# Performance work log

Measured on AMD Instinct MI355X. Metric: run time of the kernel, lower is better.

The kernel has to match this reference:

```python
import jax, jax.numpy as jnp
import numpy as np
import math

WS = 8           # window size
NUM_HEADS = 8
LN_EPS = 1e-5


def window_partition(x, ws):
    # x: [B, H, W, C] -> [B*nH*nW, ws, ws, C]
    B, H, W, C = x.shape
    x = x.reshape(B, H // ws, ws, W // ws, ws, C)
    return x.transpose(0, 1, 3, 2, 4, 5).reshape(-1, ws, ws, C)


def window_reverse(w, ws, H, W):
    # w: [B*nH*nW, ws, ws, C] -> [B, H, W, C]
    B = w.shape[0] // ((H // ws) * (W // ws))
    x = w.reshape(B, H // ws, W // ws, ws, ws, -1)
    return x.transpose(0, 1, 3, 2, 4, 5).reshape(B, H, W, -1)


def layernorm(x, g, b):
    mu = jnp.mean(x, axis=-1, keepdims=True)
    var = jnp.mean(jnp.square(x - mu), axis=-1, keepdims=True)
    return (x - mu) * jax.lax.rsqrt(var + LN_EPS) * g + b


def rotation_grid(H, W, ws):
    """Vectorized rotation_process lookup table -> sampling grid [H, W, 2]=(lat,lon)."""
    nH, nW = H // ws, W // ws
    r = 1.0 / ws
    seq = -1.0 + r + 2.0 * r * jnp.arange(ws, dtype=jnp.float32)  # make_coord centers
    ch, cw = jnp.meshgrid(seq, seq, indexing='ij')
    t0 = ch.reshape(-1) / nH                       # [ws*ws] latitude template
    t1 = cw.reshape(-1) / nW                       # [ws*ws] longitude template
    beta = (2.0 * (jnp.arange(nH, dtype=jnp.float32) + 0.5) / nH - 1.0) * (math.pi / 2)  # [nH]
    th = t0 * (math.pi / 2) + math.pi / 2
    ph = t1 * math.pi
    sb, cb = jnp.sin(beta)[:, None], jnp.cos(beta)[:, None]
    st, ct = jnp.sin(th)[None, :], jnp.cos(th)[None, :]
    sp, cp = jnp.sin(ph)[None, :], jnp.cos(ph)[None, :]
    new_th = jnp.arccos(-sb * st * cp + cb * ct)                    # [nH, ws*ws]
    new_ph = jnp.arctan2(st * sp, cb * st * cp + sb * ct)
    lat = jnp.clip((new_th - math.pi / 2) / (math.pi / 2), -1.0, 1.0)
    lon = new_ph / math.pi
    shift = 2.0 * (0.5 - (jnp.arange(nW, dtype=jnp.float32) + 0.5) / nW)
    lon = lon[:, None, :] - shift[None, :, None]                    # [nH, nW, ws*ws]
    lon = jnp.where(lon > 1.0, lon - 2.0, lon)
    lon = jnp.where(lon < -1.0, lon + 2.0, lon)
    lat = jnp.broadcast_to(lat[:, None, :], lon.shape)
    g = jnp.stack([lat, lon], axis=-1).reshape(nH, nW, ws, ws, 2)
    return g.transpose(0, 2, 1, 3, 4).reshape(H, W, 2)


def grid_sample_nearest(im, grid):
    """F.grid_sample(mode='nearest', align_corners=False, padding='zeros').
    im: [B, H, W, C]; grid: [H, W, 2]=(y,x) normalized; shared across batch."""
    B, H, W, C = im.shape
    gy, gx = grid[..., 0], grid[..., 1]
    iy = jnp.round(((gy + 1.0) * H - 1.0) / 2.0).astype(jnp.int32)
    ix = jnp.round(((gx + 1.0) * W - 1.0) / 2.0).astype(jnp.int32)
    valid = (iy >= 0) & (iy < H) & (ix >= 0) & (ix < W)
    iyc = jnp.clip(iy, 0, H - 1)
    ixc = jnp.clip(ix, 0, W - 1)
    out = im[:, iyc, ixc, :]                                        # [B, H, W, C]
    return out * valid[None, :, :, None].astype(im.dtype)


def dwconv3x3(x, w, b):
    # x: [B, C, H, W], w: [C, 1, 3, 3] depthwise
    y = jax.lax.conv_general_dilated(x, w, (1, 1), 'SAME',
                                     feature_group_count=x.shape[1],
                                     dimension_numbers=('NCHW', 'OIHW', 'NCHW'))
    return y + b[None, :, None, None]


def setup_inputs() -> dict:
    key = jax.random.key(0)
    B, H, W, C, dff = 8, 64, 128, 256, 1024
    ks = jax.random.split(key, 10)
    s = 0.02
    return {
        'x': jax.random.normal(ks[0], (B, H * W, C), jnp.float32),
        'H': H, 'W': W,
        'norm1_g': jnp.ones((C,), jnp.float32),
        'norm1_b': jnp.zeros((C,), jnp.float32),
        'wq': jax.random.normal(ks[1], (C, C), jnp.float32) * s,
        'bq': jnp.zeros((C,), jnp.float32),
        'wk': jax.random.normal(ks[2], (C, C), jnp.float32) * s,
        'bk': jnp.zeros((C,), jnp.float32),
        'wv': jax.random.normal(ks[3], (C, C), jnp.float32) * s,
        'bv': jnp.zeros((C,), jnp.float32),
        'rpe_w': jax.random.normal(ks[4], (C, 1, 3, 3), jnp.float32) * s,
        'rpe_b': jnp.zeros((C,), jnp.float32),
        'proj_w': jax.random.normal(ks[5], (C, C), jnp.float32) * s,
        'proj_b': jnp.zeros((C,), jnp.float32),
        'norm2_g': jnp.ones((C,), jnp.float32),
        'norm2_b': jnp.zeros((C,), jnp.float32),
        'fc1_w': jax.random.normal(ks[6], (C, dff), jnp.float32) * s,
        'fc1_b': jnp.zeros((dff,), jnp.float32),
        'fc2_w': jax.random.normal(ks[7], (dff, C), jnp.float32) * s,
        'fc2_b': jnp.zeros((C,), jnp.float32),
    }


def reference(x, H, W, norm1_g, norm1_b, wq, bq, wk, bk, wv, bv, rpe_w, rpe_b,
              proj_w, proj_b, norm2_g, norm2_b, fc1_w, fc1_b, fc2_w, fc2_b):
    B, L, C = x.shape
    ws, nh = WS, NUM_HEADS
    hd = C // nh
    scale = hd ** (-0.5)
    N = ws * ws

    shortcut = x
    xn = layernorm(x, norm1_g, norm1_b).reshape(B, H, W, C)
    # panoramic rotation of the key features (rotation_process)
    y = grid_sample_nearest(xn, rotation_grid(H, W, ws))

    xw = window_partition(xn, ws).reshape(-1, N, C)   # [Bw, N, C]
    yw = window_partition(y, ws).reshape(-1, N, C)
    Bw = xw.shape[0]

    q = xw @ wq + bq
    # depthwise-conv positional term on window-reversed q (rpe_table)
    qimg = window_reverse(q.reshape(-1, ws, ws, C), ws, H, W).transpose(0, 3, 1, 2)  # [B,C,H,W]
    lepe = window_partition(dwconv3x3(qimg, rpe_w, rpe_b).transpose(0, 2, 3, 1), ws).reshape(-1, N, C)

    k = yw @ wk + bk
    v = xw @ wv + bv
    qh = q.reshape(Bw, N, nh, hd).transpose(0, 2, 1, 3) * scale   # [Bw,h,N,d]
    kh = k.reshape(Bw, N, nh, hd).transpose(0, 2, 1, 3)
    vh = v.reshape(Bw, N, nh, hd).transpose(0, 2, 1, 3)
    attn = jax.nn.softmax(jnp.einsum('bhnd,bhmd->bhnm', qh, kh), axis=-1)
    out = jnp.einsum('bhnm,bhmd->bhnd', attn, vh).transpose(0, 2, 1, 3).reshape(Bw, N, C)
    out = (out + lepe) @ proj_w + proj_b

    x = shortcut + window_reverse(out.reshape(-1, ws, ws, C), ws, H, W).reshape(B, L, C)
    h = layernorm(x, norm2_g, norm2_b)
    h = jax.nn.gelu(h @ fc1_w + fc1_b, approximate=False) @ fc2_w + fc2_b
    return x + h
```

## Files before the change

### kernel.cpp

```cpp
#include <hip/hip_runtime.h>

typedef __bf16 bf16;
typedef __bf16 bf16x4 __attribute__((ext_vector_type(4)));
typedef __bf16 bf16x8 __attribute__((ext_vector_type(8)));
typedef float  f32x4  __attribute__((ext_vector_type(4)));

#define HH   64
#define WW   128
#define CC   256
#define MTOK 65536
#define PI_D 3.14159265358979323846

__device__ __forceinline__ int win_row(int b, int h, int w) {
  return ((b * 8 + (h >> 3)) * 16 + (w >> 3)) * 64 + ((h & 7) << 3) + (w & 7);
}

__device__ __forceinline__ void gl_lds16(const bf16* g, bf16* l) {
  __builtin_amdgcn_global_load_lds(
      (const __attribute__((address_space(1))) unsigned int*)g,
      (__attribute__((address_space(3))) unsigned int*)l, 16, 0, 0);
}

__device__ __forceinline__ float gelu_f(float v) {
  return 0.5f * v * (1.0f + erff(v * 0.70710678118654752f));
}

__global__ __launch_bounds__(256) void prep_kernel(
    const float* __restrict__ wq, const float* __restrict__ wk,
    const float* __restrict__ wv, const float* __restrict__ pw,
    const float* __restrict__ f1w, const float* __restrict__ f2w,
    bf16* __restrict__ wqvT, bf16* __restrict__ wkT, bf16* __restrict__ pwT,
    bf16* __restrict__ f1T, bf16* __restrict__ f2T,
    int* __restrict__ wmap, bf16* __restrict__ zrow,
    float* __restrict__ biasqv,
    const float* __restrict__ bq, const float* __restrict__ bv) {
  const int blk = blockIdx.x;
  if (blk < 768) {
    __shared__ float tile[32][33];
    const float* src; bf16* dst; int K, N, bi;
    if (blk < 64)       { src = wq;  dst = wqvT;         K = 256;  N = 256;  bi = blk;       }
    else if (blk < 128) { src = wv;  dst = wqvT + 65536; K = 256;  N = 256;  bi = blk - 64;  }
    else if (blk < 192) { src = wk;  dst = wkT;          K = 256;  N = 256;  bi = blk - 128; }
    else if (blk < 256) { src = pw;  dst = pwT;          K = 256;  N = 256;  bi = blk - 192; }
    else if (blk < 512) { src = f1w; dst = f1T;          K = 256;  N = 1024; bi = blk - 256; }
    else                { src = f2w; dst = f2T;          K = 1024; N = 256;  bi = blk - 512; }
    const int nbk = K >> 5;
    const int bk = (bi % nbk) * 32, bn = (bi / nbk) * 32;
    const int tx = threadIdx.x & 31, ty = threadIdx.x >> 5;
#pragma unroll
    for (int r = 0; r < 4; r++)
      tile[ty + 8 * r][tx] = src[(size_t)(bk + ty + 8 * r) * N + bn + tx];
    __syncthreads();
#pragma unroll
    for (int r = 0; r < 4; r++)
      dst[(size_t)(bn + ty + 8 * r) * K + bk + tx] = (bf16)tile[tx][ty + 8 * r];
    return;
  }
  int p = (blk - 768) * 256 + threadIdx.x;
  if (p < 256) zrow[p] = (bf16)0.0f;
  if (p < 512) biasqv[p] = (p < 256) ? bq[p] : bv[p - 256];
  if (p >= HH * WW) return;
  int h = p >> 7, w = p & 127;
  int bh = h >> 3, i = h & 7, bw = w >> 3, j = w & 7;
  double seq_i = -0.875 + 0.25 * i;
  double seq_j = -0.875 + 0.25 * j;
  double t0 = seq_i / 8.0, t1 = seq_j / 16.0;
  double beta = ((bh + 0.5) / 4.0 - 1.0) * (PI_D / 2.0);
  double th = t0 * (PI_D / 2.0) + PI_D / 2.0;
  double ph = t1 * PI_D;
  double sb = sin(beta), cb = cos(beta);
  double st = sin(th),  ct = cos(th);
  double sp = sin(ph),  cp = cos(ph);
  double arg = -sb * st * cp + cb * ct;
  arg = fmin(1.0, fmax(-1.0, arg));
  double nth = acos(arg);
  double nph = atan2(st * sp, cb * st * cp + sb * ct);
  double lat = (nth - PI_D / 2.0) / (PI_D / 2.0);
  lat = fmin(1.0, fmax(-1.0, lat));
  double shift = 1.0 - (2.0 * bw + 1.0) / 16.0;
  double lon = nph / PI_D - shift;
  if (lon > 1.0) lon -= 2.0; else if (lon < -1.0) lon += 2.0;
  int iy = (int)rint(((lat + 1.0) * (double)HH - 1.0) * 0.5);
  int ix = (int)rint(((lon + 1.0) * (double)WW - 1.0) * 0.5);
  bool valid = (iy >= 0 && iy < HH && ix >= 0 && ix < WW);
  int dwr = ((h >> 3) * 16 + (w >> 3)) * 64 + ((h & 7) << 3) + (w & 7);
  int src = valid ? (((iy >> 3) * 16 + (ix >> 3)) * 64 + ((iy & 7) << 3) + (ix & 7)) : -1;
  wmap[dwr] = src;
}

__global__ __launch_bounds__(256) void ln_kernel(const float* __restrict__ x,
                                                 const float* __restrict__ g,
                                                 const float* __restrict__ bta,
                                                 bf16* __restrict__ out,
                                                 int permute) {
  int token = blockIdx.x * 4 + (threadIdx.x >> 6);
  int lane = threadIdx.x & 63;
  const float4 v = *(const float4*)(x + (size_t)token * CC + lane * 4);
  float s  = v.x + v.y + v.z + v.w;
  float ss = v.x * v.x + v.y * v.y + v.z * v.z + v.w * v.w;
#pragma unroll
  for (int o = 32; o > 0; o >>= 1) {
    s  += __shfl_xor(s, o);
    ss += __shfl_xor(ss, o);
  }
  float mu = s * (1.0f / CC);
  float var = ss * (1.0f / CC) - mu * mu;
  float rs = rsqrtf(var + 1e-5f);
  int row = token;
  if (permute) {
    int b = token >> 13, l = token & 8191;
    row = win_row(b, l >> 7, l & 127);
  }
  int c = lane * 4;
  const float4 gv = *(const float4*)(g + c);
  const float4 bv = *(const float4*)(bta + c);
  bf16x4 o4;
  o4[0] = (bf16)((v.x - mu) * rs * gv.x + bv.x);
  o4[1] = (bf16)((v.y - mu) * rs * gv.y + bv.y);
  o4[2] = (bf16)((v.z - mu) * rs * gv.z + bv.z);
  o4[3] = (bf16)((v.w - mu) * rs * gv.w + bv.w);
  *(bf16x4*)(out + (size_t)row * CC + c) = o4;
}

#define EPI_BF16 0
#define EPI_GELU 1
#define EPI_PROJ 2
#define EPI_FC2  3
#define EPI_QV   4

#define TRS 72

template <int EPI, bool GATHER>
__global__ __launch_bounds__(256) void gemm_bt(const bf16* __restrict__ A,
                                               const bf16* __restrict__ Bt,
                                               const float* __restrict__ bias,
                                               bf16* __restrict__ outB,
                                               float* __restrict__ outF,
                                               const float* __restrict__ res,
                                               const int* __restrict__ amap,
                                               const bf16* __restrict__ zrow,
                                               bf16* __restrict__ outB2,
                                               int M, int N, int K) {
  __shared__ bf16 lA[128 * 32];
  __shared__ bf16 lB[128 * 32];
  __shared__ bf16 trV[(EPI == EPI_QV) ? 4 * 64 * TRS : 4];
  const int t = threadIdx.x;
  const int wave = t >> 6, lane = t & 63;
  const int quad = lane >> 4, l16 = lane & 15;
  const int mb = blockIdx.x, nb = blockIdx.y;
  const int wm = wave >> 1, wn = wave & 1;

  f32x4 acc[4][4];
#pragma unroll
  for (int i = 0; i < 4; i++)
#pragma unroll
    for (int j = 0; j < 4; j++)
#pragma unroll
      for (int r = 0; r < 4; r++) acc[i][j][r] = 0.0f;

  const int arow = t >> 2;
  const int acol = (t & 3) << 3;
  const bf16 *gA, *gA2;
  if (GATHER) {
    int r1 = mb * 128 + arow;
    int b1 = r1 >> 13, s1 = amap[r1 & 8191];
    gA = (s1 >= 0) ? A + ((size_t)((b1 << 13) + s1)) * K + acol : zrow + acol;
    int r2 = r1 + 64;
    int b2 = r2 >> 13, s2 = amap[r2 & 8191];
    gA2 = (s2 >= 0) ? A + ((size_t)((b2 << 13) + s2)) * K + acol : zrow + acol;
  } else {
    gA = A + (size_t)(mb * 128 + arow) * K + acol;
    gA2 = gA + (size_t)64 * K;
  }
  const bf16* gB  = Bt + (size_t)(nb * 128 + arow) * K + acol;
  const bf16* gB2 = gB + (size_t)64 * K;
  bf16* lAp  = &lA[t * 8];
  bf16* lBp  = &lB[t * 8];
  bf16* lAp2 = &lA[2048 + t * 8];
  bf16* lBp2 = &lB[2048 + t * 8];

  for (int kk = 0; kk < K; kk += 32) {
    __syncthreads();
    gl_lds16(gA + kk, lAp);
    gl_lds16(gA2 + kk, lAp2);
    gl_lds16(gB + kk, lBp);
    gl_lds16(gB2 + kk, lBp2);
    __syncthreads();
    bf16x8 af[4], bfr[4];
#pragma unroll
    for (int i = 0; i < 4; i++)
      af[i] = *(const bf16x8*)&lA[(wm * 64 + i * 16 + l16) * 32 + quad * 8];
#pragma unroll
    for (int j = 0; j < 4; j++)
      bfr[j] = *(const bf16x8*)&lB[(wn * 64 + j * 16 + l16) * 32 + quad * 8];
#pragma unroll
    for (int i = 0; i < 4; i++)
#pragma unroll
      for (int j = 0; j < 4; j++)
        acc[i][j] = __builtin_amdgcn_mfma_f32_16x16x32_bf16(af[i], bfr[j], acc[i][j], 0, 0, 0);
  }

  const int m0 = mb * 128 + wm * 64;
  const int n0 = nb * 128 + wn * 64;

  if (EPI == EPI_QV && nb >= 2) {
    bf16* tw = &trV[wave * 64 * TRS];
#pragma unroll
    for (int i = 0; i < 4; i++)
#pragma unroll
      for (int j = 0; j < 4; j++) {
        const float bsv = bias[n0 + j * 16 + l16];
        bf16x4 pk;
#pragma unroll
        for (int r = 0; r < 4; r++) pk[r] = (bf16)(acc[i][j][r] + bsv);
        *(bf16x4*)&tw[(j * 16 + l16) * TRS + i * 16 + quad * 4] = pk;
      }
    const int win = mb * 2 + wm;
    const int chbase = n0 - 256;
#pragma unroll
    for (int s = 0; s < 8; s++) {
      const int ch = s * 8 + (lane >> 3);
      const int tk = (lane & 7) * 8;
      bf16x8 vv = *(const bf16x8*)&tw[ch * TRS + tk];
      *(bf16x8*)(outB2 + ((size_t)win * 256 + chbase + ch) * 64 + tk) = vv;
    }
  } else {
#pragma unroll
    for (int i = 0; i < 4; i++) {
#pragma unroll
      for (int j = 0; j < 4; j++) {
        const int col = n0 + j * 16 + l16;
        const int rowb = m0 + i * 16 + quad * 4;
        const float bsv = bias[col];
#pragma unroll
        for (int r = 0; r < 4; r++) {
          const int row = rowb + r;
          float v = acc[i][j][r] + bsv;
          if (EPI == EPI_BF16) {
            outB[(size_t)row * N + col] = (bf16)v;
          } else if (EPI == EPI_QV) {
            outB[(size_t)row * 256 + col] = (bf16)v;
          } else if (EPI == EPI_GELU) {
            outB[(size_t)row * N + col] = (bf16)gelu_f(v);
          } else if (EPI == EPI_FC2) {
            size_t idx = (size_t)row * N + col;
            outF[idx] = res[idx] + v;
          } else {
            int wi = row >> 6, tt = row & 63;
            int b = wi >> 7, hb = (wi >> 4) & 7, wb = wi & 15;
            int h = hb * 8 + (tt >> 3), w = wb * 8 + (tt & 7);
            size_t idx = ((size_t)(b * 8192 + h * 128 + w)) * 256 + col;
            outF[idx] = res[idx] + v;
          }
        }
      }
    }
  }
}

__global__ __launch_bounds__(256) void lepe_kernel(const bf16* __restrict__ qb,
                                                   const float* __restrict__ rw,
                                                   const float* __restrict__ rb,
                                                   bf16* __restrict__ ao) {
  __shared__ __align__(16) bf16 hq[100 * 256];
  const int blk = blockIdx.x;
  const int b = blk >> 7, hb = (blk >> 4) & 7, wb = blk & 15;
  const int t = threadIdx.x;
  const int h0 = hb * 8 - 1, w0 = wb * 8 - 1;

  for (int idx = t; idx < 3200; idx += 256) {
    int pix = idx >> 5, ch = (idx & 31) * 8;
    int pi = pix / 10, pj = pix - pi * 10;
    int h = h0 + pi, w = w0 + pj;
    bf16x8 val;
#pragma unroll
    for (int e = 0; e < 8; e++) val[e] = (bf16)0.0f;
    if (h >= 0 && h < HH && w >= 0 && w < WW)
      val = *(const bf16x8*)(qb + (size_t)win_row(b, h, w) * 256 + ch);
    *(bf16x8*)(&hq[pix * 256 + ch]) = val;
  }
  __syncthreads();

  const int cg = t & 31, c0 = cg * 8;
  const int i = t >> 5;

  float wr[9][8];
#pragma unroll
  for (int e = 0; e < 8; e++)
#pragma unroll
    for (int tap = 0; tap < 9; tap++) wr[tap][e] = rw[(c0 + e) * 9 + tap];
  float bias[8];
  *(float4*)&bias[0] = *(const float4*)(rb + c0);
  *(float4*)&bias[4] = *(const float4*)(rb + c0 + 4);

  float cur[3][3][8];
#pragma unroll
  for (int rr = 0; rr < 3; rr++)
#pragma unroll
    for (int cc = 0; cc < 2; cc++) {
      bf16x8 v = *(const bf16x8*)(&hq[((i + rr) * 10 + cc) * 256 + c0]);
#pragma unroll
      for (int e = 0; e < 8; e++) cur[rr][cc][e] = (float)v[e];
    }

#pragma unroll
  for (int j = 0; j < 8; j++) {
    const int snew = (j + 2) % 3;
#pragma unroll
    for (int rr = 0; rr < 3; rr++) {
      bf16x8 v = *(const bf16x8*)(&hq[((i + rr) * 10 + (j + 2)) * 256 + c0]);
#pragma unroll
      for (int e = 0; e < 8; e++) cur[rr][snew][e] = (float)v[e];
    }
    float acc[8];
#pragma unroll
    for (int e = 0; e < 8; e++) acc[e] = bias[e];
#pragma unroll
    for (int rr = 0; rr < 3; rr++)
#pragma unroll
      for (int dc = 0; dc < 3; dc++) {
        const int slot = (j + dc) % 3;
        const int tap = rr * 3 + dc;
#pragma unroll
        for (int e = 0; e < 8; e++) acc[e] += cur[rr][slot][e] * wr[tap][e];
      }
    bf16x8 o;
#pragma unroll
    for (int e = 0; e < 8; e++) o[e] = (bf16)acc[e];
    *(bf16x8*)(ao + (size_t)(blk * 64 + i * 8 + j) * 256 + c0) = o;
  }
}

#define SP 74

__global__ __launch_bounds__(256) void attn_kernel(const bf16* __restrict__ qb,
                                                   const bf16* __restrict__ kb,
                                                   const bf16* __restrict__ vt,
                                                   bf16* __restrict__ ao) {
  __shared__ __align__(16) bf16 Pl[4][64 * SP];
  const int wave = threadIdx.x >> 6, lane = threadIdx.x & 63;
  const int quad = lane >> 4, l16 = lane & 15;
  const int win = blockIdx.x >> 1;
  const size_t rowbase = (size_t)win * 64;
  const int head = ((blockIdx.x & 1) << 2) + wave;
  const int hc = head * 32;
  bf16* P = Pl[wave];
  const float scale = 0.17677669529663687f;

  bf16x8 aq[4], bk4[4];
#pragma unroll
  for (int mi = 0; mi < 4; mi++)
    aq[mi] = *(const bf16x8*)(qb + (rowbase + mi * 16 + l16) * 256 + hc + quad * 8);
#pragma unroll
  for (int ni = 0; ni < 4; ni++)
    bk4[ni] = *(const bf16x8*)(kb + (rowbase + ni * 16 + l16) * 256 + hc + quad * 8);
  f32x4 sacc[4][4];
#pragma unroll
  for (int mi = 0; mi < 4; mi++)
#pragma unroll
    for (int ni = 0; ni < 4; ni++)
#pragma unroll
      for (int r = 0; r < 4; r++) sacc[mi][ni][r] = 0.0f;
#pragma unroll
  for (int mi = 0; mi < 4; mi++)
#pragma unroll
    for (int ni = 0; ni < 4; ni++)
      sacc[mi][ni] = __builtin_amdgcn_mfma_f32_16x16x32_bf16(aq[mi], bk4[ni], sacc[mi][ni], 0, 0, 0);

  bf16x8 vb2[2][2];
#pragma unroll
  for (int n0 = 0; n0 < 2; n0++)
#pragma unroll
    for (int kc = 0; kc < 2; kc++)
      vb2[n0][kc] = *(const bf16x8*)(vt + ((size_t)win * 256 + hc + n0 * 16 + l16) * 64 +
                                     kc * 32 + quad * 8);

#pragma unroll
  for (int mi = 0; mi < 4; mi++) {
#pragma unroll
    for (int r = 0; r < 4; r++) {
      float mx = -1e30f;
#pragma unroll
      for (int ni = 0; ni < 4; ni++) mx = fmaxf(mx, sacc[mi][ni][r]);
      mx = fmaxf(mx, __shfl_xor(mx, 1));
      mx = fmaxf(mx, __shfl_xor(mx, 2));
      mx = fmaxf(mx, __shfl_xor(mx, 4));
      mx = fmaxf(mx, __shfl_xor(mx, 8));
      float sm = 0.0f;
#pragma unroll
      for (int ni = 0; ni < 4; ni++) {
        float e = expf(scale * (sacc[mi][ni][r] - mx));
        sacc[mi][ni][r] = e;
        sm += e;
      }
      sm += __shfl_xor(sm, 1);
      sm += __shfl_xor(sm, 2);
      sm += __shfl_xor(sm, 4);
      sm += __shfl_xor(sm, 8);
      float inv = 1.0f / sm;
#pragma unroll
      for (int ni = 0; ni < 4; ni++) sacc[mi][ni][r] *= inv;
    }
#pragma unroll
    for (int ni = 0; ni < 4; ni++)
#pragma unroll
      for (int r = 0; r < 4; r++)
        P[(mi * 16 + quad * 4 + r) * SP + ni * 16 + l16] = (bf16)sacc[mi][ni][r];
  }

  f32x4 oacc[4][2];
#pragma unroll
  for (int mi = 0; mi < 4; mi++)
#pragma unroll
    for (int n0 = 0; n0 < 2; n0++)
#pragma unroll
      for (int r = 0; r < 4; r++) oacc[mi][n0][r] = 0.0f;
#pragma unroll
  for (int mi = 0; mi < 4; mi++)
#pragma unroll
    for (int kc = 0; kc < 2; kc++) {
      bf16x8 pf = *(const bf16x8*)&P[(mi * 16 + l16) * SP + kc * 32 + quad * 8];
#pragma unroll
      for (int n0 = 0; n0 < 2; n0++)
        oacc[mi][n0] = __builtin_amdgcn_mfma_f32_16x16x32_bf16(pf, vb2[n0][kc], oacc[mi][n0], 0, 0, 0);
    }

  bf16* Ol = P;
#pragma unroll
  for (int mi = 0; mi < 4; mi++)
#pragma unroll
    for (int n0 = 0; n0 < 2; n0++)
#pragma unroll
      for (int r = 0; r < 4; r++)
        Ol[(mi * 16 + quad * 4 + r) * 34 + n0 * 16 + l16] = (bf16)oacc[mi][n0][r];

  bf16* aop = ao + (rowbase + lane) * 256 + hc;
#pragma unroll
  for (int cc = 0; cc < 4; cc++) {
    bf16x8 ov = *(const bf16x8*)&Ol[lane * 34 + cc * 8];
    bf16x8 lp = *(const bf16x8*)(aop + cc * 8);
    bf16x8 so;
#pragma unroll
    for (int e = 0; e < 8; e++) so[e] = (bf16)((float)ov[e] + (float)lp[e]);
    *(bf16x8*)(aop + cc * 8) = so;
  }
}

extern "C" void kernel_launch(void* const* d_in, const int* in_sizes, int n_in,
                              void* d_out, int out_size, void* d_ws, size_t ws_size,
                              hipStream_t stream) {
  const float* x     = (const float*)d_in[0];
  const float* n1g   = (const float*)d_in[3];
  const float* n1b   = (const float*)d_in[4];
  const float* wq    = (const float*)d_in[5];
  const float* bq    = (const float*)d_in[6];
  const float* wk    = (const float*)d_in[7];
  const float* bk    = (const float*)d_in[8];
  const float* wv    = (const float*)d_in[9];
  const float* bv    = (const float*)d_in[10];
  const float* rpe_w = (const float*)d_in[11];
  const float* rpe_b = (const float*)d_in[12];
  const float* pw    = (const float*)d_in[13];
  const float* pb    = (const float*)d_in[14];
  const float* n2g   = (const float*)d_in[15];
  const float* n2b   = (const float*)d_in[16];
  const float* f1w   = (const float*)d_in[17];
  const float* f1b   = (const float*)d_in[18];
  const float* f2w   = (const float*)d_in[19];
  const float* f2b   = (const float*)d_in[20];
  float* out = (float*)d_out;
  char* ws = (char*)d_ws;

  const size_t A_ = 33554432ull;
  bf16* xw  = (bf16*)(ws);
  bf16* ao  = (bf16*)(ws);
  bf16* xh  = (bf16*)(ws);
  bf16* qb  = (bf16*)(ws + A_);
  bf16* vt  = (bf16*)(ws + 2 * A_);
  bf16* h1  = (bf16*)(ws + A_);
  bf16* kb  = (bf16*)d_out;
  char* wsp = ws + 3 * A_;
  bf16* wqvT = (bf16*)(wsp);
  bf16* wkT  = (bf16*)(wsp + 262144);
  bf16* pwT  = (bf16*)(wsp + 393216);
  bf16* f1T  = (bf16*)(wsp + 524288);
  bf16* f2T  = (bf16*)(wsp + 1048576);
  float* biasqv = (float*)(wsp + 1572864);
  int*   wmap   = (int*)(wsp + 1574912);
  bf16*  zrow   = (bf16*)(wsp + 1607680);

  prep_kernel<<<800, 256, 0, stream>>>(wq, wk, wv, pw, f1w, f2w,
                                       wqvT, wkT, pwT, f1T, f2T,
                                       wmap, zrow, biasqv, bq, bv);

  ln_kernel<<<MTOK / 4, 256, 0, stream>>>(x, n1g, n1b, xw, 1);

  gemm_bt<EPI_QV, false><<<dim3(512, 4), 256, 0, stream>>>(
      xw, wqvT, biasqv, qb, nullptr, nullptr, nullptr, nullptr, vt, MTOK, 512, 256);
  gemm_bt<EPI_BF16, true><<<dim3(512, 2), 256, 0, stream>>>(
      xw, wkT, bk, kb, nullptr, nullptr, wmap, zrow, nullptr, MTOK, 256, 256);

  lepe_kernel<<<1024, 256, 0, stream>>>(qb, rpe_w, rpe_b, ao);
  attn_kernel<<<2048, 256, 0, stream>>>(qb, kb, vt, ao);

  gemm_bt<EPI_PROJ, false><<<dim3(512, 2), 256, 0, stream>>>(
      ao, pwT, pb, nullptr, out, x, nullptr, nullptr, nullptr, MTOK, 256, 256);

  ln_kernel<<<MTOK / 4, 256, 0, stream>>>(out, n2g, n2b, xh, 0);

  const int CH = 32768;
  for (int c = 0; c < 2; c++) {
    gemm_bt<EPI_GELU, false><<<dim3(CH / 128, 8), 256, 0, stream>>>(
        xh + (size_t)c * CH * 256, f1T, f1b, h1, nullptr, nullptr, nullptr, nullptr, nullptr,
        CH, 1024, 256);
    gemm_bt<EPI_FC2, false><<<dim3(CH / 128, 2), 256, 0, stream>>>(
        h1, f2T, f2b, nullptr, out + (size_t)c * CH * 256, out + (size_t)c * CH * 256,
        nullptr, nullptr, nullptr, CH, 256, 1024);
  }
}
```

Before: 486.5 us.

## Load GEMM operands directly from global memory and fuse Q/V/K projection launches

Replaces the LDS-staged GEMM, which used global_load_lds and two barriers per K step, with kernels where each wave loads its MFMA fragments straight from global memory into registers. The K projection with its gathered rows is merged into the Q/V projection as extra grid columns, so one launch covers all three. This removes LDS traffic and barrier stalls, but each wave now fetches fragments with no reuse across waves in the block. That means more global and L2 traffic, plus short strided loads.

```diff
diff --git a/kernel.cpp b/kernel.cpp
--- a/kernel.cpp
+++ b/kernel.cpp
@@ -13,12 +13,6 @@
 
 __device__ __forceinline__ int win_row(int b, int h, int w) {
   return ((b * 8 + (h >> 3)) * 16 + (w >> 3)) * 64 + ((h & 7) << 3) + (w & 7);
-}
-
-__device__ __forceinline__ void gl_lds16(const bf16* g, bf16* l) {
-  __builtin_amdgcn_global_load_lds(
-      (const __attribute__((address_space(1))) unsigned int*)g,
-      (__attribute__((address_space(3))) unsigned int*)l, 16, 0, 0);
 }
 
 __device__ __forceinline__ float gelu_f(float v) {
@@ -122,33 +116,116 @@
   *(bf16x4*)(out + (size_t)row * CC + c) = o4;
 }
 
-#define EPI_BF16 0
 #define EPI_GELU 1
 #define EPI_PROJ 2
 #define EPI_FC2  3
-#define EPI_QV   4
+
+template <int EPI, int KT>
+__global__ __launch_bounds__(256) void gemm_dir(const bf16* __restrict__ A,
+                                                const bf16* __restrict__ Bt,
+                                                const float* __restrict__ bias,
+                                                bf16* __restrict__ outB,
+                                                float* __restrict__ outF,
+                                                const float* __restrict__ res,
+                                                int N) {
+  const int K = KT * 32;
+  const int lane = threadIdx.x & 63, wave = threadIdx.x >> 6;
+  const int quad = lane >> 4, l16 = lane & 15;
+  const int mb = blockIdx.x, nb = blockIdx.y;
+  const int wm = wave >> 1, wn = wave & 1;
+
+  const bf16* ap = A  + (size_t)(mb * 128 + wm * 64 + l16) * K + quad * 8;
+  const bf16* bp = Bt + (size_t)(nb * 128 + wn * 64 + l16) * K + quad * 8;
+
+  f32x4 acc[4][4];
+#pragma unroll
+  for (int i = 0; i < 4; i++)
+#pragma unroll
+    for (int j = 0; j < 4; j++)
+#pragma unroll
+      for (int r = 0; r < 4; r++) acc[i][j][r] = 0.0f;
+
+  constexpr int UN = (KT > 8) ? 4 : KT;
+  for (int ko = 0; ko < KT / UN; ko++) {
+#pragma unroll
+    for (int ku = 0; ku < UN; ku++) {
+      const int kc = ko * UN + ku;
+      bf16x8 af[4], bfr[4];
+#pragma unroll
+      for (int i = 0; i < 4; i++)
+        af[i] = *(const bf16x8*)(ap + (size_t)i * 16 * K + kc * 32);
+#pragma unroll
+      for (int j = 0; j < 4; j++)
+        bfr[j] = *(const bf16x8*)(bp + (size_t)j * 16 * K + kc * 32);
+#pragma unroll
+      for (int i = 0; i < 4; i++)
+#pragma unroll
+        for (int j = 0; j < 4; j++)
+          acc[i][j] = __builtin_amdgcn_mfma_f32_16x16x32_bf16(af[i], bfr[j], acc[i][j], 0, 0, 0);
+    }
+  }
+
+  const int m0 = mb * 128 + wm * 64;
+  const int n0 = nb * 128 + wn * 64;
+#pragma unroll
+  for (int i = 0; i < 4; i++) {
+#pragma unroll
+    for (int j = 0; j < 4; j++) {
+      const int col = n0 + j * 16 + l16;
+      const int rowb = m0 + i * 16 + quad * 4;
+      const float bsv = bias[col];
+#pragma unroll
+      for (int r = 0; r < 4; r++) {
+        const int row = rowb + r;
+        float v = acc[i][j][r] + bsv;
+        if (EPI == EPI_GELU) {
+          outB[(size_t)row * N + col] = (bf16)gelu_f(v);
+        } else if (EPI == EPI_FC2) {
+          size_t idx = (size_t)row * N + col;
+          outF[idx] = res[idx] + v;
+        } else {
+          int wi = row >> 6, tt = row & 63;
+          int b = wi >> 7, hb = (wi >> 4) & 7, wb = wi & 15;
+          int h = hb * 8 + (tt >> 3), w = wb * 8 + (tt & 7);
+          size_t idx = ((size_t)(b * 8192 + h * 128 + w)) * 256 + col;
+          outF[idx] = res[idx] + v;
+        }
+      }
+    }
+  }
+}
 
 #define TRS 72
 
-template <int EPI, bool GATHER>
-__global__ __launch_bounds__(256) void gemm_bt(const bf16* __restrict__ A,
-                                               const bf16* __restrict__ Bt,
-                                               const float* __restrict__ bias,
-                                               bf16* __restrict__ outB,
-                                               float* __restrict__ outF,
-                                               const float* __restrict__ res,
-                                               const int* __restrict__ amap,
-                                               const bf16* __restrict__ zrow,
-                                               bf16* __restrict__ outB2,
-                                               int M, int N, int K) {
-  __shared__ bf16 lA[128 * 32];
-  __shared__ bf16 lB[128 * 32];
-  __shared__ bf16 trV[(EPI == EPI_QV) ? 4 * 64 * TRS : 4];
+__global__ __launch_bounds__(256) void gemm_qvk(
+    const bf16* __restrict__ xw, const bf16* __restrict__ wqvT,
+    const bf16* __restrict__ wkT, const float* __restrict__ biasqv,
+    const float* __restrict__ bk, bf16* __restrict__ qb,
+    bf16* __restrict__ vt, bf16* __restrict__ kb,
+    const int* __restrict__ wmap, const bf16* __restrict__ zrow) {
+  __shared__ __align__(16) bf16 trV[4 * 64 * TRS];
   const int t = threadIdx.x;
   const int wave = t >> 6, lane = t & 63;
   const int quad = lane >> 4, l16 = lane & 15;
   const int mb = blockIdx.x, nb = blockIdx.y;
   const int wm = wave >> 1, wn = wave & 1;
+  const bool isK = (nb >= 4);
+
+  const bf16* ap[4];
+#pragma unroll
+  for (int i = 0; i < 4; i++) {
+    int r1 = mb * 128 + wm * 64 + i * 16 + l16;
+    if (isK) {
+      int s = wmap[r1 & 8191];
+      ap[i] = (s >= 0) ? xw + ((size_t)((r1 & ~8191) + s)) * 256 + quad * 8
+                       : zrow + quad * 8;
+    } else {
+      ap[i] = xw + (size_t)r1 * 256 + quad * 8;
+    }
+  }
+  const int nloc = isK ? (nb - 4) : nb;
+  const bf16* Bt = isK ? wkT : wqvT;
+  const bf16* bp = Bt + (size_t)(nloc * 128 + wn * 64 + l16) * 256 + quad * 8;
 
   f32x4 acc[4][4];
 #pragma unroll
@@ -158,41 +235,15 @@
 #pragma unroll
       for (int r = 0; r < 4; r++) acc[i][j][r] = 0.0f;
 
-  const int arow = t >> 2;
-  const int acol = (t & 3) << 3;
-  const bf16 *gA, *gA2;
-  if (GATHER) {
-    int r1 = mb * 128 + arow;
-    int b1 = r1 >> 13, s1 = amap[r1 & 8191];
-    gA = (s1 >= 0) ? A + ((size_t)((b1 << 13) + s1)) * K + acol : zrow + acol;
-    int r2 = r1 + 64;
-    int b2 = r2 >> 13, s2 = amap[r2 & 8191];
-    gA2 = (s2 >= 0) ? A + ((size_t)((b2 << 13) + s2)) * K + acol : zrow + acol;
-  } else {
-    gA = A + (size_t)(mb * 128 + arow) * K + acol;
-    gA2 = gA + (size_t)64 * K;
-  }
-  const bf16* gB  = Bt + (size_t)(nb * 128 + arow) * K + acol;
-  const bf16* gB2 = gB + (size_t)64 * K;
-  bf16* lAp  = &lA[t * 8];
-  bf16* lBp  = &lB[t * 8];
-  bf16* lAp2 = &lA[2048 + t * 8];
-  bf16* lBp2 = &lB[2048 + t * 8];
-
-  for (int kk = 0; kk < K; kk += 32) {
-    __syncthreads();
-    gl_lds16(gA + kk, lAp);
-    gl_lds16(gA2 + kk, lAp2);
-    gl_lds16(gB + kk, lBp);
-    gl_lds16(gB2 + kk, lBp2);
-    __syncthreads();
+#pragma unroll
+  for (int kc = 0; kc < 8; kc++) {
     bf16x8 af[4], bfr[4];
 #pragma unroll
     for (int i = 0; i < 4; i++)
-      af[i] = *(const bf16x8*)&lA[(wm * 64 + i * 16 + l16) * 32 + quad * 8];
+      af[i] = *(const bf16x8*)(ap[i] + kc * 32);
 #pragma unroll
     for (int j = 0; j < 4; j++)
-      bfr[j] = *(const bf16x8*)&lB[(wn * 64 + j * 16 + l16) * 32 + quad * 8];
+      bfr[j] = *(const bf16x8*)(bp + (size_t)j * 16 * 256 + kc * 32);
 #pragma unroll
     for (int i = 0; i < 4; i++)
 #pragma unroll
@@ -201,58 +252,42 @@
   }
 
   const int m0 = mb * 128 + wm * 64;
-  const int n0 = nb * 128 + wn * 64;
-
-  if (EPI == EPI_QV && nb >= 2) {
+
+  if (!isK && nb >= 2) {
+    const int n0g = nb * 128 + wn * 64;
     bf16* tw = &trV[wave * 64 * TRS];
 #pragma unroll
     for (int i = 0; i < 4; i++)
 #pragma unroll
       for (int j = 0; j < 4; j++) {
-        const float bsv = bias[n0 + j * 16 + l16];
+        const float bsv = biasqv[n0g + j * 16 + l16];
         bf16x4 pk;
 #pragma unroll
         for (int r = 0; r < 4; r++) pk[r] = (bf16)(acc[i][j][r] + bsv);
         *(bf16x4*)&tw[(j * 16 + l16) * TRS + i * 16 + quad * 4] = pk;
       }
     const int win = mb * 2 + wm;
-    const int chbase = n0 - 256;
+    const int chbase = n0g - 256;
 #pragma unroll
     for (int s = 0; s < 8; s++) {
       const int ch = s * 8 + (lane >> 3);
       const int tk = (lane & 7) * 8;
       bf16x8 vv = *(const bf16x8*)&tw[ch * TRS + tk];
-      *(bf16x8*)(outB2 + ((size_t)win * 256 + chbase + ch) * 64 + tk) = vv;
+      *(bf16x8*)(vt + ((size_t)win * 256 + chbase + ch) * 64 + tk) = vv;
     }
   } else {
+    const int n0l = nloc * 128 + wn * 64;
+    bf16* outp = isK ? kb : qb;
 #pragma unroll
     for (int i = 0; i < 4; i++) {
 #pragma unroll
       for (int j = 0; j < 4; j++) {
-        const int col = n0 + j * 16 + l16;
+        const int col = n0l + j * 16 + l16;
+        const float bsv = isK ? bk[col] : biasqv[col];
         const int rowb = m0 + i * 16 + quad * 4;
-        const float bsv = bias[col];
-#pragma unroll
-        for (int r = 0; r < 4; r++) {
-          const int row = rowb + r;
-          float v = acc[i][j][r] + bsv;
-          if (EPI == EPI_BF16) {
-            outB[(size_t)row * N + col] = (bf16)v;
-          } else if (EPI == EPI_QV) {
-            outB[(size_t)row * 256 + col] = (bf16)v;
-          } else if (EPI == EPI_GELU) {
-            outB[(size_t)row * N + col] = (bf16)gelu_f(v);
-          } else if (EPI == EPI_FC2) {
-            size_t idx = (size_t)row * N + col;
-            outF[idx] = res[idx] + v;
-          } else {
-            int wi = row >> 6, tt = row & 63;
-            int b = wi >> 7, hb = (wi >> 4) & 7, wb = wi & 15;
-            int h = hb * 8 + (tt >> 3), w = wb * 8 + (tt & 7);
-            size_t idx = ((size_t)(b * 8192 + h * 128 + w)) * 256 + col;
-            outF[idx] = res[idx] + v;
-          }
-        }
+#pragma unroll
+        for (int r = 0; r < 4; r++)
+          outp[(size_t)(rowb + r) * 256 + col] = (bf16)(acc[i][j][r] + bsv);
       }
     }
   }
@@ -495,26 +530,22 @@
 
   ln_kernel<<<MTOK / 4, 256, 0, stream>>>(x, n1g, n1b, xw, 1);
 
-  gemm_bt<EPI_QV, false><<<dim3(512, 4), 256, 0, stream>>>(
-      xw, wqvT, biasqv, qb, nullptr, nullptr, nullptr, nullptr, vt, MTOK, 512, 256);
-  gemm_bt<EPI_BF16, true><<<dim3(512, 2), 256, 0, stream>>>(
-      xw, wkT, bk, kb, nullptr, nullptr, wmap, zrow, nullptr, MTOK, 256, 256);
+  gemm_qvk<<<dim3(512, 6), 256, 0, stream>>>(xw, wqvT, wkT, biasqv, bk,
+                                             qb, vt, kb, wmap, zrow);
 
   lepe_kernel<<<1024, 256, 0, stream>>>(qb, rpe_w, rpe_b, ao);
   attn_kernel<<<2048, 256, 0, stream>>>(qb, kb, vt, ao);
 
-  gemm_bt<EPI_PROJ, false><<<dim3(512, 2), 256, 0, stream>>>(
-      ao, pwT, pb, nullptr, out, x, nullptr, nullptr, nullptr, MTOK, 256, 256);
+  gemm_dir<EPI_PROJ, 8><<<dim3(512, 2), 256, 0, stream>>>(
+      ao, pwT, pb, nullptr, out, x, 256);
 
   ln_kernel<<<MTOK / 4, 256, 0, stream>>>(out, n2g, n2b, xh, 0);
 
   const int CH = 32768;
   for (int c = 0; c < 2; c++) {
-    gemm_bt<EPI_GELU, false><<<dim3(CH / 128, 8), 256, 0, stream>>>(
-        xh + (size_t)c * CH * 256, f1T, f1b, h1, nullptr, nullptr, nullptr, nullptr, nullptr,
-        CH, 1024, 256);
-    gemm_bt<EPI_FC2, false><<<dim3(CH / 128, 2), 256, 0, stream>>>(
-        h1, f2T, f2b, nullptr, out + (size_t)c * CH * 256, out + (size_t)c * CH * 256,
-        nullptr, nullptr, nullptr, CH, 256, 1024);
-  }
-}
+    gemm_dir<EPI_GELU, 8><<<dim3(CH / 128, 8), 256, 0, stream>>>(
+        xh + (size_t)c * CH * 256, f1T, f1b, h1, nullptr, nullptr, 1024);
+    gemm_dir<EPI_FC2, 32><<<dim3(CH / 128, 2), 256, 0, stream>>>(
+        h1, f2T, f2b, nullptr, out + (size_t)c * CH * 256, out + (size_t)c * CH * 256, 256);
+  }
+}
```

Measured after the change: 678.1 us. 1.39x slower.
